# Kernel tuning notes

Measured on AMD Instinct MI355X. Metric: run time of the kernel, lower is better.

Reference implementation:

```python
import jax, jax.numpy as jnp
import numpy as np

# mamba-130m backbone dims. NOTE: the original torch code wires Conv1d(1,8,...) into a
# 768-d Mamba (a latent bug); we resolve it by making the downsample conv emit d_model.
B, L_IN = 2, 135000
D_MODEL, N_LAYERS = 768, 24
D_INNER, D_STATE, D_CONV, DT_RANK = 1536, 16, 4, 48
K_DS, S_DS = 32, 32
LATENT = 64


def setup_inputs() -> dict:
    key = jax.random.key(0)
    ks = jax.random.split(key, 16)
    s = 0.02
    dt = jax.random.uniform(ks[12], (N_LAYERS, D_INNER), minval=1e-3, maxval=1e-1)
    return {
        "x": jax.random.normal(ks[0], (B, 1, L_IN), dtype=jnp.float32),
        "conv_w": jax.random.normal(ks[1], (D_MODEL, 1, K_DS)) * s,
        "conv_b": jnp.zeros((D_MODEL,)),
        "norm_w": jnp.ones((N_LAYERS, D_MODEL)),
        "in_proj_w": jax.random.normal(ks[2], (N_LAYERS, 2 * D_INNER, D_MODEL)) * s,
        "conv1d_w": jax.random.normal(ks[3], (N_LAYERS, D_INNER, D_CONV)) * s,
        "conv1d_b": jnp.zeros((N_LAYERS, D_INNER)),
        "x_proj_w": jax.random.normal(ks[4], (N_LAYERS, DT_RANK + 2 * D_STATE, D_INNER)) * s,
        "dt_proj_w": jax.random.normal(ks[5], (N_LAYERS, D_INNER, DT_RANK)) * s,
        "dt_proj_b": dt + jnp.log(-jnp.expm1(-dt)),  # inverse-softplus init
        "A_log": jnp.log(jnp.broadcast_to(jnp.arange(1, D_STATE + 1, dtype=jnp.float32), (N_LAYERS, D_INNER, D_STATE)) + 0.0),
        "D_skip": jnp.ones((N_LAYERS, D_INNER)),
        "out_proj_w": jax.random.normal(ks[6], (N_LAYERS, D_MODEL, D_INNER)) * s,
        "norm_f_w": jnp.ones((D_MODEL,)),
        "proj_w": jax.random.normal(ks[7], (LATENT, D_MODEL)) * s,
        "proj_b": jnp.zeros((LATENT,)),
        "ln_w": jnp.ones((LATENT,)),
        "ln_b": jnp.zeros((LATENT,)),
    }


def _rmsnorm(x, w):
    return x * jax.lax.rsqrt(jnp.mean(x * x, axis=-1, keepdims=True) + 1e-5) * w


def _mamba_layer(h, p):
    norm_w, in_w, cw, cb, xp_w, dt_w, dt_b, A_log, Dp, out_w = p
    xz = jnp.einsum('btd,ed->bte', _rmsnorm(h, norm_w), in_w)  # e = 2*d_inner
    u, z = jnp.split(xz, 2, axis=-1)
    # causal depthwise conv over time
    uc = jax.lax.conv_general_dilated(jnp.transpose(u, (0, 2, 1)), cw[:, None, :], (1,),
                                      [(D_CONV - 1, 0)], dimension_numbers=('NCH', 'OIH', 'NCH'),
                                      feature_group_count=D_INNER)
    u = jax.nn.silu(jnp.transpose(uc + cb[None, :, None], (0, 2, 1)))  # (B,T,d_inner)
    proj = jnp.einsum('btd,ed->bte', u, xp_w)
    dt, Bm, Cm = jnp.split(proj, [DT_RANK, DT_RANK + D_STATE], axis=-1)
    delta = jax.nn.softplus(jnp.einsum('btr,dr->btd', dt, dt_w) + dt_b)
    A = -jnp.exp(A_log)  # (d_inner, d_state)

    def step(hc, inp):
        u_t, d_t, b_t, c_t = inp  # (B,d_inner),(B,d_inner),(B,d_state),(B,d_state)
        hc = jnp.exp(d_t[..., None] * A) * hc + (d_t * u_t)[..., None] * b_t[:, None, :]
        return hc, jnp.einsum('bds,bs->bd', hc, c_t)

    h0 = jnp.zeros((u.shape[0], D_INNER, D_STATE), dtype=u.dtype)
    tfirst = lambda a: jnp.transpose(a, (1, 0, 2))
    _, ys = jax.lax.scan(step, h0, (tfirst(u), tfirst(delta), tfirst(Bm), tfirst(Cm)))
    y = (jnp.transpose(ys, (1, 0, 2)) + u * Dp) * jax.nn.silu(z)
    return h + jnp.einsum('bte,de->btd', y, out_w), None


def _forward(x, conv_w, conv_b, norm_w, in_proj_w, conv1d_w, conv1d_b, x_proj_w, dt_proj_w,
             dt_proj_b, A_log, D_skip, out_proj_w, norm_f_w, proj_w, proj_b, ln_w, ln_b):
    # downsample: (B,1,135000) -> (B,768,4218) -> (B,4218,768)
    xds = jax.lax.conv_general_dilated(x, conv_w, (S_DS,), 'VALID',
                                       dimension_numbers=('NCH', 'OIH', 'NCH')) + conv_b[None, :, None]
    h = jnp.transpose(xds, (0, 2, 1))
    params = (norm_w, in_proj_w, conv1d_w, conv1d_b, x_proj_w, dt_proj_w, dt_proj_b, A_log, D_skip, out_proj_w)
    h, _ = jax.lax.scan(_mamba_layer, h, params)
    h = _rmsnorm(h, norm_f_w)  # last_hidden_state
    pooled = h.mean(axis=1)  # mean pooling
    zed = pooled @ proj_w.T + proj_b
    mu = zed.mean(-1, keepdims=True)
    var = ((zed - mu) ** 2).mean(-1, keepdims=True)
    return (zed - mu) * jax.lax.rsqrt(var + 1e-5) * ln_w + ln_b  # dropout is identity in eval


def reference(x, conv_w, conv_b, norm_w, in_proj_w, conv1d_w, conv1d_b, x_proj_w, dt_proj_w,
              dt_proj_b, A_log, D_skip, out_proj_w, norm_f_w, proj_w, proj_b, ln_w, ln_b):
    return _forward(x, conv_w, conv_b, norm_w, in_proj_w, conv1d_w, conv1d_b, x_proj_w,
                    dt_proj_w, dt_proj_b, A_log, D_skip, out_proj_w, norm_f_w, proj_w,
                    proj_b, ln_w, ln_b)
```

## Files before the change

### kernel.cpp

```cpp
#include <hip/hip_runtime.h>
#include <hip/hip_bf16.h>
#include <math.h>

#define TT 4218
#define BB 2
#define DM 768
#define DI 1536
#define DS 16
#define DTR 48
#define LC 64
#define NCHUNK 66
#define ROWS (BB*TT)
#define NLAYER 24

typedef short short8 __attribute__((ext_vector_type(8)));
typedef float f32x4 __attribute__((ext_vector_type(4)));

__device__ __forceinline__ float silu_f(float x) { return x / (1.0f + __expf(-x)); }
__device__ __forceinline__ float softplus_f(float x) {
  return (x > 15.0f) ? x : log1pf(__expf(x));
}
__device__ __forceinline__ unsigned short f2bf(float x) {
  unsigned int u = __float_as_uint(x);
  u = (u + 0x7fffu + ((u >> 16) & 1u)) >> 16;
  return (unsigned short)u;
}
__device__ __forceinline__ float bf2f(unsigned short s) {
  return __uint_as_float(((unsigned int)s) << 16);
}

__global__ __launch_bounds__(256)
void k_f2bf(const float4* __restrict__ in, ushort4* __restrict__ out, int n4) {
  int i = blockIdx.x*256 + threadIdx.x;
  if (i >= n4) return;
  float4 v = in[i];
  ushort4 o;
  o.x = f2bf(v.x); o.y = f2bf(v.y); o.z = f2bf(v.z); o.w = f2bf(v.w);
  out[i] = o;
}

__global__ __launch_bounds__(256)
void k_cvt_dtw(const float* __restrict__ in, unsigned short* __restrict__ out, int n) {
  int i = blockIdx.x*256 + threadIdx.x;
  if (i >= n) return;
  int col = i & 63, row = i >> 6;
  out[i] = (col < DTR) ? f2bf(in[row*DTR + col]) : (unsigned short)0;
}

__global__ __launch_bounds__(256)
void k_zero_dtpad(unsigned short* __restrict__ fdt) {
  int i = blockIdx.x*256 + threadIdx.x;
  if (i >= ROWS*16) return;
  int r = i >> 4, c = i & 15;
  fdt[(size_t)r*64 + DTR + c] = 0;
}

__global__ __launch_bounds__(256)
void k_conv_ds(const float* __restrict__ x, const float* __restrict__ cw,
               const float* __restrict__ cb, float* __restrict__ h) {
  int bt = blockIdx.x;
  int b = bt / TT, t = bt % TT;
  __shared__ float xs[32];
  int tid = threadIdx.x;
  if (tid < 32) xs[tid] = x[(size_t)b*135000 + (size_t)t*32 + tid];
  __syncthreads();
  for (int d = tid; d < DM; d += 256) {
    float s = cb[d];
    const float* w = cw + d*32;
    #pragma unroll
    for (int k = 0; k < 32; ++k) s = fmaf(xs[k], w[k], s);
    h[(size_t)bt*DM + d] = s;
  }
}

__global__ __launch_bounds__(256)
void k_rmsnorm(const float* __restrict__ in, const float* __restrict__ w,
               unsigned short* __restrict__ out) {
  int row = blockIdx.x, tid = threadIdx.x;
  const float* xp = in + (size_t)row*DM;
  float v0 = xp[tid], v1 = xp[tid+256], v2 = xp[tid+512];
  float ss = v0*v0 + v1*v1 + v2*v2;
  #pragma unroll
  for (int off = 32; off > 0; off >>= 1) ss += __shfl_down(ss, off, 64);
  __shared__ float sred[4];
  if ((tid & 63) == 0) sred[tid >> 6] = ss;
  __syncthreads();
  float tot = sred[0] + sred[1] + sred[2] + sred[3];
  float sc = rsqrtf(tot * (1.0f/DM) + 1e-5f);
  unsigned short* op = out + (size_t)row*DM;
  op[tid]     = f2bf(v0*sc*w[tid]);
  op[tid+256] = f2bf(v1*sc*w[tid+256]);
  op[tid+512] = f2bf(v2*sc*w[tid+512]);
}

#define GLL(g, l) __builtin_amdgcn_global_load_lds( \
    (const __attribute__((address_space(1))) void*)(g), \
    (__attribute__((address_space(3))) void*)(l), 16, 0, 0)

template<int MODE>
__global__ __launch_bounds__(256)
void k_gemm_bf(const unsigned short* __restrict__ A,
               const unsigned short* __restrict__ W,
               const float* __restrict__ bias,
               float* __restrict__ Cf,
               unsigned short* __restrict__ Cb0, unsigned short* __restrict__ Cb1,
               int ldc, int M, int N, int K) {
  __shared__ unsigned short As[128*32];
  __shared__ unsigned short Ws[128*32];
  const int tid = threadIdx.x;
  const int m0 = blockIdx.x*128, n0 = blockIdx.y*128;
  const int lane = tid & 63;
  const int wave = tid >> 6;
  const int wm = (wave >> 1)*64, wn = (wave & 1)*64;

  const int sA = tid & 3;
  const int r0 = tid >> 2;
  const int r1 = r0 + 64;
  const int seg0 = sA ^ ((r0 >> 1) & 3);
  const int seg1 = sA ^ ((r1 >> 1) & 3);
  const unsigned short* gA0 = A + (size_t)min(m0+r0, M-1)*K + seg0*8;
  const unsigned short* gA1 = A + (size_t)min(m0+r1, M-1)*K + seg1*8;
  const unsigned short* gW0 = W + (size_t)min(n0+r0, N-1)*K + seg0*8;
  const unsigned short* gW1 = W + (size_t)min(n0+r1, N-1)*K + seg1*8;
  unsigned short* lA0 = As + tid*8;
  unsigned short* lA1 = As + (tid+256)*8;
  unsigned short* lW0 = Ws + tid*8;
  unsigned short* lW1 = Ws + (tid+256)*8;

  f32x4 acc[4][4];
  #pragma unroll
  for (int i = 0; i < 4; ++i)
    #pragma unroll
    for (int j = 0; j < 4; ++j) acc[i][j] = (f32x4){0.f,0.f,0.f,0.f};

  const int lr = lane & 15, kg = lane >> 4;
  const int sw = (kg ^ ((lr >> 1) & 3)) * 8;
  const int aoff = (wm + lr)*32 + sw;
  const int boff = (wn + lr)*32 + sw;

  for (int k0 = 0; k0 < K; k0 += 32) {
    GLL(gA0, lA0); GLL(gA1, lA1);
    GLL(gW0, lW0); GLL(gW1, lW1);
    gA0 += 32; gA1 += 32; gW0 += 32; gW1 += 32;
    __syncthreads();
    short8 af[4], bfr[4];
    #pragma unroll
    for (int i = 0; i < 4; ++i) {
      af[i]  = *(const short8*)(As + aoff + i*512);
      bfr[i] = *(const short8*)(Ws + boff + i*512);
    }
    #pragma unroll
    for (int i = 0; i < 4; ++i)
      #pragma unroll
      for (int j = 0; j < 4; ++j)
        acc[i][j] = __builtin_amdgcn_mfma_f32_16x16x32_bf16(af[i], bfr[j], acc[i][j], 0, 0, 0);
    __syncthreads();
  }

  #pragma unroll
  for (int i = 0; i < 4; ++i) {
    int gr0 = m0 + wm + i*16 + kg*4;
    #pragma unroll
    for (int j = 0; j < 4; ++j) {
      int gc = n0 + wn + j*16 + lr;
      if (gc >= N) continue;
      #pragma unroll
      for (int r = 0; r < 4; ++r) {
        int gr = gr0 + r;
        if (gr >= M) continue;
        float v = acc[i][j][r];
        if (MODE == 0) {
          if (gc < DI) Cb0[(size_t)gr*ldc + gc] = f2bf(v);
          else         Cb1[(size_t)gr*ldc + gc - DI] = f2bf(v);
        } else if (MODE == 1) {
          Cf[(size_t)gr*ldc + gc] += v;
        } else {
          Cf[(size_t)gr*ldc + gc] = softplus_f(v + bias[gc]);
        }
      }
    }
  }
}

__global__ __launch_bounds__(256)
void k_gemm_xp(const unsigned short* __restrict__ A,
               const unsigned short* __restrict__ W,
               float* __restrict__ Cpr, unsigned short* __restrict__ Cdt,
               int M) {
  __shared__ unsigned short As[64*32];
  __shared__ unsigned short Ws[80*32];
  const int tid = threadIdx.x;
  const int m0 = blockIdx.x*64;
  const int lane = tid & 63;
  const int wave = tid >> 6;
  const int K = DI;

  const int rA = tid >> 2;
  const int segA = (tid & 3) ^ ((rA >> 1) & 3);
  const unsigned short* gA = A + (size_t)min(m0+rA, M-1)*K + segA*8;
  unsigned short* lA = As + tid*8;
  const int rW0 = tid >> 2;
  const int segW0 = (tid & 3) ^ ((rW0 >> 1) & 3);
  const unsigned short* gW0 = W + (size_t)rW0*K + segW0*8;
  unsigned short* lW0 = Ws + tid*8;
  const int idx1 = tid + 256;
  const int rW1 = idx1 >> 2;
  const int segW1 = (idx1 & 3) ^ ((rW1 >> 1) & 3);
  const unsigned short* gW1 = W + (size_t)min(rW1,79)*K + segW1*8;
  unsigned short* lW1 = Ws + (size_t)idx1*8;

  f32x4 acc[5];
  #pragma unroll
  for (int j = 0; j < 5; ++j) acc[j] = (f32x4){0.f,0.f,0.f,0.f};

  const int lr = lane & 15, kg = lane >> 4;
  const int sw = (kg ^ ((lr >> 1) & 3)) * 8;
  const int aoff = (wave*16 + lr)*32 + sw;

  for (int k0 = 0; k0 < K; k0 += 32) {
    GLL(gA, lA);
    GLL(gW0, lW0);
    if (wave == 0) GLL(gW1, lW1);
    gA += 32; gW0 += 32; gW1 += 32;
    __syncthreads();
    short8 af = *(const short8*)(As + aoff);
    #pragma unroll
    for (int j = 0; j < 5; ++j) {
      short8 bf = *(const short8*)(Ws + (j*16 + lr)*32 + sw);
      acc[j] = __builtin_amdgcn_mfma_f32_16x16x32_bf16(af, bf, acc[j], 0, 0, 0);
    }
    __syncthreads();
  }

  #pragma unroll
  for (int j = 0; j < 5; ++j) {
    int gc = j*16 + lr;
    #pragma unroll
    for (int r = 0; r < 4; ++r) {
      int gr = m0 + wave*16 + kg*4 + r;
      if (gr >= M) continue;
      float v = acc[j][r];
      Cpr[(size_t)gr*80 + gc] = v;
      if (gc < DTR) Cdt[(size_t)gr*64 + gc] = f2bf(v);
    }
  }
}

__global__ __launch_bounds__(256)
void k_dwconv(const unsigned short* __restrict__ U0, const float* __restrict__ cw,
              const float* __restrict__ cb, unsigned short* __restrict__ ubf) {
  size_t i = (size_t)blockIdx.x*256 + threadIdx.x;
  if (i >= (size_t)ROWS*DI) return;
  int d = (int)(i % DI);
  long bt = (long)(i / DI);
  int t = (int)(bt % TT);
  float s = cb[d];
  #pragma unroll
  for (int k = 0; k < 4; ++k) {
    int tt = t - 3 + k;
    if (tt >= 0) s = fmaf(bf2f(U0[(size_t)(bt - 3 + k)*DI + d]), cw[d*4 + k], s);
  }
  ubf[i] = f2bf(silu_f(s));
}

__global__ __launch_bounds__(256)
void k_scan1(const float* __restrict__ delta, const unsigned short* __restrict__ u,
             const float* __restrict__ proj, const float* __restrict__ A_log,
             float* __restrict__ P, float* __restrict__ H) {
  int c = blockIdx.x, b = blockIdx.z;
  int d = blockIdx.y * 256 + threadIdx.x;
  float A[DS];
  #pragma unroll
  for (int s = 0; s < DS; ++s) A[s] = -__expf(A_log[d*DS + s]);
  float h[DS] = {};
  float Pp[DS];
  #pragma unroll
  for (int s = 0; s < DS; ++s) Pp[s] = 1.0f;
  int t0 = c * LC, t1 = min(t0 + LC, TT);
  for (int t = t0; t < t1; ++t) {
    size_t bt = (size_t)b*TT + t;
    float dl = delta[bt*DI + d];
    float du = dl * bf2f(u[bt*DI + d]);
    const float* pbm = proj + bt*80 + DTR;
    #pragma unroll
    for (int s = 0; s < DS; ++s) {
      float e = __expf(dl * A[s]);
      Pp[s] *= e;
      h[s] = fmaf(e, h[s], du * pbm[s]);
    }
  }
  size_t o = (((size_t)c*BB + b)*DI + d)*DS;
  #pragma unroll
  for (int s = 0; s < DS; ++s) { P[o+s] = Pp[s]; H[o+s] = h[s]; }
}

__global__ __launch_bounds__(256)
void k_scan2(float* __restrict__ P, float* __restrict__ H) {
  int i = blockIdx.x*256 + threadIdx.x;
  const int CH = BB*DI*DS;
  float carry = 0.0f;
  for (int c = 0; c < NCHUNK; ++c) {
    size_t o = (size_t)c*CH + i;
    float p = P[o], h0 = H[o];
    H[o] = carry;
    carry = fmaf(p, carry, h0);
  }
}

__global__ __launch_bounds__(256)
void k_scan3(const float* __restrict__ delta, const unsigned short* __restrict__ u,
             const unsigned short* __restrict__ z, const float* __restrict__ proj,
             const float* __restrict__ A_log, const float* __restrict__ Dskip,
             const float* __restrict__ H, unsigned short* __restrict__ y) {
  int c = blockIdx.x, b = blockIdx.z;
  int d = blockIdx.y * 256 + threadIdx.x;
  float A[DS];
  #pragma unroll
  for (int s = 0; s < DS; ++s) A[s] = -__expf(A_log[d*DS + s]);
  float h[DS];
  size_t o = (((size_t)c*BB + b)*DI + d)*DS;
  #pragma unroll
  for (int s = 0; s < DS; ++s) h[s] = H[o+s];
  float Dd = Dskip[d];
  int t0 = c * LC, t1 = min(t0 + LC, TT);
  for (int t = t0; t < t1; ++t) {
    size_t bt = (size_t)b*TT + t;
    float dl = delta[bt*DI + d];
    float uu = bf2f(u[bt*DI + d]);
    float du = dl * uu;
    const float* pbm = proj + bt*80 + DTR;
    const float* pcm = pbm + DS;
    float yt = 0.0f;
    #pragma unroll
    for (int s = 0; s < DS; ++s) {
      float e = __expf(dl * A[s]);
      h[s] = fmaf(e, h[s], du * pbm[s]);
      yt = fmaf(h[s], pcm[s], yt);
    }
    float zz = bf2f(z[bt*DI + d]);
    y[bt*DI + d] = f2bf((yt + uu*Dd) * silu_f(zz));
  }
}

__global__ __launch_bounds__(256)
void k_poolpart(const unsigned short* __restrict__ hn, float* __restrict__ pp) {
  int seg = blockIdx.x, b = blockIdx.z;
  int d = blockIdx.y*256 + threadIdx.x;
  int t0 = seg*132, t1 = min(t0 + 132, TT);
  float s = 0.0f;
  for (int t = t0; t < t1; ++t) s += bf2f(hn[((size_t)b*TT + t)*DM + d]);
  pp[((size_t)b*32 + seg)*DM + d] = s;
}

__global__ __launch_bounds__(256)
void k_head(const float* __restrict__ pp, const float* __restrict__ pw,
            const float* __restrict__ pb, const float* __restrict__ lnw,
            const float* __restrict__ lnb, float* __restrict__ out) {
  int b = blockIdx.x, tid = threadIdx.x;
  __shared__ float pooled[DM];
  for (int d = tid; d < DM; d += 256) {
    float s = 0.0f;
    for (int seg = 0; seg < 32; ++seg) s += pp[((size_t)b*32 + seg)*DM + d];
    pooled[d] = s * (1.0f/(float)TT);
  }
  __syncthreads();
  __shared__ float zed[64];
  if (tid < 64) {
    float s = pb[tid];
    const float* w = pw + (size_t)tid*DM;
    for (int d = 0; d < DM; ++d) s = fmaf(pooled[d], w[d], s);
    zed[tid] = s;
  }
  __syncthreads();
  __shared__ float mv[2];
  if (tid == 0) {
    float mu = 0.0f;
    for (int l = 0; l < 64; ++l) mu += zed[l];
    mu *= (1.0f/64.0f);
    float var = 0.0f;
    for (int l = 0; l < 64; ++l) { float dd = zed[l]-mu; var += dd*dd; }
    var *= (1.0f/64.0f);
    mv[0] = mu; mv[1] = rsqrtf(var + 1e-5f);
  }
  __syncthreads();
  if (tid < 64) out[b*64 + tid] = (zed[tid]-mv[0])*mv[1]*lnw[tid] + lnb[tid];
}

extern "C" void kernel_launch(void* const* d_in, const int* in_sizes, int n_in,
                              void* d_out, int out_size, void* d_ws, size_t ws_size,
                              hipStream_t stream) {
  (void)in_sizes; (void)n_in; (void)out_size; (void)ws_size;
  const float* x    = (const float*)d_in[0];
  const float* cw   = (const float*)d_in[1];
  const float* cb   = (const float*)d_in[2];
  const float* nw   = (const float*)d_in[3];
  const float* inw  = (const float*)d_in[4];
  const float* c1w  = (const float*)d_in[5];
  const float* c1b  = (const float*)d_in[6];
  const float* xpw  = (const float*)d_in[7];
  const float* dtw  = (const float*)d_in[8];
  const float* dtb  = (const float*)d_in[9];
  const float* alog = (const float*)d_in[10];
  const float* dsk  = (const float*)d_in[11];
  const float* outw = (const float*)d_in[12];
  const float* nfw  = (const float*)d_in[13];
  const float* pw   = (const float*)d_in[14];
  const float* pb   = (const float*)d_in[15];
  const float* lnw  = (const float*)d_in[16];
  const float* lnb  = (const float*)d_in[17];

  char* wsb = (char*)d_ws;
  size_t o = 0;
  float* f_h  = (float*)(wsb + o); o += (size_t)ROWS*DM*4;
  float* f_pr = (float*)(wsb + o); o += (size_t)ROWS*80*4;
  float* f_dl = (float*)(wsb + o); o += (size_t)ROWS*DI*4;
  float* f_P  = (float*)(wsb + o); o += (size_t)NCHUNK*BB*DI*DS*4;
  float* f_H  = (float*)(wsb + o); o += (size_t)NCHUNK*BB*DI*DS*4;
  float* f_pp = (float*)(wsb + o); o += (size_t)BB*32*DM*4;
  unsigned short* hn_bf = (unsigned short*)(wsb + o); o += (size_t)ROWS*DM*2;
  unsigned short* u0_bf = (unsigned short*)(wsb + o); o += (size_t)ROWS*DI*2;
  unsigned short* z_bf  = (unsigned short*)(wsb + o); o += (size_t)ROWS*DI*2;
  unsigned short* u_bf  = (unsigned short*)(wsb + o); o += (size_t)ROWS*DI*2;
  unsigned short* y_bf  = (unsigned short*)(wsb + o); o += (size_t)ROWS*DI*2;
  unsigned short* f_dt  = (unsigned short*)(wsb + o); o += (size_t)ROWS*64*2;
  unsigned short* w_in  = (unsigned short*)(wsb + o); o += (size_t)2*DI*DM*2;
  unsigned short* w_xp  = (unsigned short*)(wsb + o); o += (size_t)NLAYER*80*DI*2;
  unsigned short* w_out = (unsigned short*)(wsb + o); o += (size_t)NLAYER*DM*DI*2;
  unsigned short* w_dt  = (unsigned short*)(wsb + o); o += (size_t)NLAYER*DI*64*2;

  k_conv_ds<<<ROWS, 256, 0, stream>>>(x, cw, cb, f_h);
  k_f2bf<<<(NLAYER*80*DI/4+255)/256, 256, 0, stream>>>(
      (const float4*)xpw, (ushort4*)w_xp, NLAYER*80*DI/4);
  k_f2bf<<<(NLAYER*DM*DI/4+255)/256, 256, 0, stream>>>(
      (const float4*)outw, (ushort4*)w_out, NLAYER*DM*DI/4);
  k_cvt_dtw<<<(NLAYER*DI*64+255)/256, 256, 0, stream>>>(dtw, w_dt, NLAYER*DI*64);
  k_zero_dtpad<<<(ROWS*16+255)/256, 256, 0, stream>>>(f_dt);

  for (int lay = 0; lay < NLAYER; ++lay) {
    k_f2bf<<<(2*DI*DM/4+255)/256, 256, 0, stream>>>(
        (const float4*)(inw + (size_t)lay*2*DI*DM), (ushort4*)w_in, 2*DI*DM/4);
    k_rmsnorm<<<ROWS, 256, 0, stream>>>(f_h, nw + (size_t)lay*DM, hn_bf);
    k_gemm_bf<0><<<dim3(66,24), 256, 0, stream>>>(
        hn_bf, w_in, nullptr, nullptr, u0_bf, z_bf, DI, ROWS, 2*DI, DM);
    k_dwconv<<<((size_t)ROWS*DI+255)/256, 256, 0, stream>>>(
        u0_bf, c1w + (size_t)lay*DI*4, c1b + (size_t)lay*DI, u_bf);
    k_gemm_xp<<<132, 256, 0, stream>>>(
        u_bf, w_xp + (size_t)lay*80*DI, f_pr, f_dt, ROWS);
    k_gemm_bf<2><<<dim3(66,12), 256, 0, stream>>>(
        f_dt, w_dt + (size_t)lay*DI*64, dtb + (size_t)lay*DI,
        f_dl, nullptr, nullptr, DI, ROWS, DI, 64);
    k_scan1<<<dim3(NCHUNK,6,BB), 256, 0, stream>>>(
        f_dl, u_bf, f_pr, alog + (size_t)lay*DI*DS, f_P, f_H);
    k_scan2<<<dim3((BB*DI*DS)/256), 256, 0, stream>>>(f_P, f_H);
    k_scan3<<<dim3(NCHUNK,6,BB), 256, 0, stream>>>(
        f_dl, u_bf, z_bf, f_pr, alog + (size_t)lay*DI*DS,
        dsk + (size_t)lay*DI, f_H, y_bf);
    k_gemm_bf<1><<<dim3(66,6), 256, 0, stream>>>(
        y_bf, w_out + (size_t)lay*DM*DI, nullptr,
        f_h, nullptr, nullptr, DM, ROWS, DM, DI);
  }

  k_rmsnorm<<<ROWS, 256, 0, stream>>>(f_h, nfw, hn_bf);
  k_poolpart<<<dim3(32,3,BB), 256, 0, stream>>>(hn_bf, f_pp);
  k_head<<<BB, 256, 0, stream>>>(f_pp, pw, pb, lnw, lnb, (float*)d_out);
}
```

Before: 11.12 ms.

## Vectorize scan and dwconv loads, widen xp GEMM K-tile, pad GEMM grids

Several unrelated micro-optimizations land together. The dwconv kernel now handles four channels per thread with vector loads, the scan kernels read B/C/A_log/H as float4, scan1 computes the chunk decay as exp(sum(dt)*A) instead of a running product, scan2 prefetches two chunks ahead, and the x_proj GEMM uses a 64-wide K tile with an 8-way XOR swizzle. The GEMM grids are enlarged to 72 row-blocks with an early exit for out-of-range blocks. The intent is fewer memory instructions and fewer barrier iterations, at the cost of more LDS in the xp GEMM and a slightly different rounding of the chunk decay.

```diff
diff --git a/kernel.cpp b/kernel.cpp
--- a/kernel.cpp
+++ b/kernel.cpp
@@ -105,10 +105,11 @@
                float* __restrict__ Cf,
                unsigned short* __restrict__ Cb0, unsigned short* __restrict__ Cb1,
                int ldc, int M, int N, int K) {
+  const int m0 = blockIdx.x*128, n0 = blockIdx.y*128;
+  if (m0 >= M) return;
   __shared__ unsigned short As[128*32];
   __shared__ unsigned short Ws[128*32];
   const int tid = threadIdx.x;
-  const int m0 = blockIdx.x*128, n0 = blockIdx.y*128;
   const int lane = tid & 63;
   const int wave = tid >> 6;
   const int wm = (wave >> 1)*64, wn = (wave & 1)*64;
@@ -187,47 +188,54 @@
                const unsigned short* __restrict__ W,
                float* __restrict__ Cpr, unsigned short* __restrict__ Cdt,
                int M) {
-  __shared__ unsigned short As[64*32];
-  __shared__ unsigned short Ws[80*32];
+  __shared__ unsigned short As[64*64];
+  __shared__ unsigned short Ws[80*64];
   const int tid = threadIdx.x;
   const int m0 = blockIdx.x*64;
   const int lane = tid & 63;
   const int wave = tid >> 6;
   const int K = DI;
 
-  const int rA = tid >> 2;
-  const int segA = (tid & 3) ^ ((rA >> 1) & 3);
-  const unsigned short* gA = A + (size_t)min(m0+rA, M-1)*K + segA*8;
-  unsigned short* lA = As + tid*8;
-  const int rW0 = tid >> 2;
-  const int segW0 = (tid & 3) ^ ((rW0 >> 1) & 3);
-  const unsigned short* gW0 = W + (size_t)rW0*K + segW0*8;
+  const int rA0 = tid >> 3,        gA0s = (tid & 7) ^ (rA0 & 7);
+  const int rA1 = (tid+256) >> 3,  gA1s = ((tid+256) & 7) ^ (rA1 & 7);
+  const unsigned short* gA0 = A + (size_t)min(m0+rA0, M-1)*K + gA0s*8;
+  const unsigned short* gA1 = A + (size_t)min(m0+rA1, M-1)*K + gA1s*8;
+  unsigned short* lA0 = As + tid*8;
+  unsigned short* lA1 = As + (size_t)(tid+256)*8;
+  const int rW0 = tid >> 3,        gW0s = (tid & 7) ^ (rW0 & 7);
+  const int rW1 = (tid+256) >> 3,  gW1s = ((tid+256) & 7) ^ (rW1 & 7);
+  const int rW2 = (tid+512) >> 3,  gW2s = ((tid+512) & 7) ^ (rW2 & 7);
+  const unsigned short* gW0 = W + (size_t)rW0*K + gW0s*8;
+  const unsigned short* gW1 = W + (size_t)rW1*K + gW1s*8;
+  const unsigned short* gW2 = W + (size_t)min(rW2,79)*K + gW2s*8;
   unsigned short* lW0 = Ws + tid*8;
-  const int idx1 = tid + 256;
-  const int rW1 = idx1 >> 2;
-  const int segW1 = (idx1 & 3) ^ ((rW1 >> 1) & 3);
-  const unsigned short* gW1 = W + (size_t)min(rW1,79)*K + segW1*8;
-  unsigned short* lW1 = Ws + (size_t)idx1*8;
+  unsigned short* lW1 = Ws + (size_t)(tid+256)*8;
+  unsigned short* lW2 = Ws + (size_t)(tid+512)*8;
+  const bool doW2 = (tid < 128);
 
   f32x4 acc[5];
   #pragma unroll
   for (int j = 0; j < 5; ++j) acc[j] = (f32x4){0.f,0.f,0.f,0.f};
 
   const int lr = lane & 15, kg = lane >> 4;
-  const int sw = (kg ^ ((lr >> 1) & 3)) * 8;
-  const int aoff = (wave*16 + lr)*32 + sw;
-
-  for (int k0 = 0; k0 < K; k0 += 32) {
-    GLL(gA, lA);
-    GLL(gW0, lW0);
-    if (wave == 0) GLL(gW1, lW1);
-    gA += 32; gW0 += 32; gW1 += 32;
+  const int rowA = wave*16 + lr;
+
+  for (int k0 = 0; k0 < K; k0 += 64) {
+    GLL(gA0, lA0); GLL(gA1, lA1);
+    GLL(gW0, lW0); GLL(gW1, lW1);
+    if (doW2) GLL(gW2, lW2);
+    gA0 += 64; gA1 += 64; gW0 += 64; gW1 += 64; gW2 += 64;
     __syncthreads();
-    short8 af = *(const short8*)(As + aoff);
-    #pragma unroll
-    for (int j = 0; j < 5; ++j) {
-      short8 bf = *(const short8*)(Ws + (j*16 + lr)*32 + sw);
-      acc[j] = __builtin_amdgcn_mfma_f32_16x16x32_bf16(af, bf, acc[j], 0, 0, 0);
+    #pragma unroll
+    for (int ks = 0; ks < 2; ++ks) {
+      const int G = ks*4 + kg;
+      short8 af = *(const short8*)(As + ((size_t)rowA*8 + (G ^ (rowA & 7)))*8);
+      #pragma unroll
+      for (int j = 0; j < 5; ++j) {
+        const int rw = j*16 + lr;
+        short8 bf = *(const short8*)(Ws + ((size_t)rw*8 + (G ^ (rw & 7)))*8);
+        acc[j] = __builtin_amdgcn_mfma_f32_16x16x32_bf16(af, bf, acc[j], 0, 0, 0);
+      }
     }
     __syncthreads();
   }
@@ -249,18 +257,36 @@
 __global__ __launch_bounds__(256)
 void k_dwconv(const unsigned short* __restrict__ U0, const float* __restrict__ cw,
               const float* __restrict__ cb, unsigned short* __restrict__ ubf) {
-  size_t i = (size_t)blockIdx.x*256 + threadIdx.x;
-  if (i >= (size_t)ROWS*DI) return;
-  int d = (int)(i % DI);
-  long bt = (long)(i / DI);
+  size_t i4 = (size_t)blockIdx.x*256 + threadIdx.x;
+  if (i4 >= (size_t)ROWS*DI/4) return;
+  size_t base = i4*4;
+  int d = (int)(base % DI);
+  size_t bt = base / DI;
   int t = (int)(bt % TT);
-  float s = cb[d];
+  float4 cbv = *(const float4*)(cb + d);
+  float s0 = cbv.x, s1 = cbv.y, s2 = cbv.z, s3 = cbv.w;
+  float4 w0v = *(const float4*)(cw + (size_t)(d+0)*4);
+  float4 w1v = *(const float4*)(cw + (size_t)(d+1)*4);
+  float4 w2v = *(const float4*)(cw + (size_t)(d+2)*4);
+  float4 w3v = *(const float4*)(cw + (size_t)(d+3)*4);
+  const float* w0 = (const float*)&w0v;
+  const float* w1 = (const float*)&w1v;
+  const float* w2 = (const float*)&w2v;
+  const float* w3 = (const float*)&w3v;
   #pragma unroll
   for (int k = 0; k < 4; ++k) {
     int tt = t - 3 + k;
-    if (tt >= 0) s = fmaf(bf2f(U0[(size_t)(bt - 3 + k)*DI + d]), cw[d*4 + k], s);
-  }
-  ubf[i] = f2bf(silu_f(s));
+    if (tt < 0) continue;
+    ushort4 uu = *(const ushort4*)(U0 + (bt - 3 + k)*DI + d);
+    s0 = fmaf(bf2f(uu.x), w0[k], s0);
+    s1 = fmaf(bf2f(uu.y), w1[k], s1);
+    s2 = fmaf(bf2f(uu.z), w2[k], s2);
+    s3 = fmaf(bf2f(uu.w), w3[k], s3);
+  }
+  ushort4 o4;
+  o4.x = f2bf(silu_f(s0)); o4.y = f2bf(silu_f(s1));
+  o4.z = f2bf(silu_f(s2)); o4.w = f2bf(silu_f(s3));
+  *(ushort4*)(ubf + base) = o4;
 }
 
 __global__ __launch_bounds__(256)
@@ -270,40 +296,60 @@
   int c = blockIdx.x, b = blockIdx.z;
   int d = blockIdx.y * 256 + threadIdx.x;
   float A[DS];
-  #pragma unroll
-  for (int s = 0; s < DS; ++s) A[s] = -__expf(A_log[d*DS + s]);
+  {
+    const float4* a4 = (const float4*)(A_log + (size_t)d*DS);
+    #pragma unroll
+    for (int q = 0; q < 4; ++q) {
+      float4 v = a4[q];
+      A[q*4+0] = -__expf(v.x); A[q*4+1] = -__expf(v.y);
+      A[q*4+2] = -__expf(v.z); A[q*4+3] = -__expf(v.w);
+    }
+  }
   float h[DS] = {};
-  float Pp[DS];
-  #pragma unroll
-  for (int s = 0; s < DS; ++s) Pp[s] = 1.0f;
+  float sdl = 0.0f;
   int t0 = c * LC, t1 = min(t0 + LC, TT);
   for (int t = t0; t < t1; ++t) {
     size_t bt = (size_t)b*TT + t;
     float dl = delta[bt*DI + d];
     float du = dl * bf2f(u[bt*DI + d]);
-    const float* pbm = proj + bt*80 + DTR;
+    const float4* pb4 = (const float4*)(proj + bt*80 + DTR);
+    float4 B0 = pb4[0], B1 = pb4[1], B2 = pb4[2], B3 = pb4[3];
+    float Bv[DS] = {B0.x,B0.y,B0.z,B0.w, B1.x,B1.y,B1.z,B1.w,
+                    B2.x,B2.y,B2.z,B2.w, B3.x,B3.y,B3.z,B3.w};
+    sdl += dl;
     #pragma unroll
     for (int s = 0; s < DS; ++s) {
       float e = __expf(dl * A[s]);
-      Pp[s] *= e;
-      h[s] = fmaf(e, h[s], du * pbm[s]);
+      h[s] = fmaf(e, h[s], du * Bv[s]);
     }
   }
   size_t o = (((size_t)c*BB + b)*DI + d)*DS;
   #pragma unroll
-  for (int s = 0; s < DS; ++s) { P[o+s] = Pp[s]; H[o+s] = h[s]; }
+  for (int q = 0; q < 4; ++q) {
+    float4 pv, hv;
+    pv.x = __expf(sdl*A[q*4+0]); pv.y = __expf(sdl*A[q*4+1]);
+    pv.z = __expf(sdl*A[q*4+2]); pv.w = __expf(sdl*A[q*4+3]);
+    hv.x = h[q*4+0]; hv.y = h[q*4+1]; hv.z = h[q*4+2]; hv.w = h[q*4+3];
+    *(float4*)(P + o + q*4) = pv;
+    *(float4*)(H + o + q*4) = hv;
+  }
 }
 
 __global__ __launch_bounds__(256)
 void k_scan2(float* __restrict__ P, float* __restrict__ H) {
   int i = blockIdx.x*256 + threadIdx.x;
-  const int CH = BB*DI*DS;
+  const size_t CH = (size_t)BB*DI*DS;
+  size_t o = (size_t)i;
   float carry = 0.0f;
+  float p0 = P[o],      h0 = H[o];
+  float p1 = P[o + CH], h1 = H[o + CH];
   for (int c = 0; c < NCHUNK; ++c) {
-    size_t o = (size_t)c*CH + i;
-    float p = P[o], h0 = H[o];
+    float p2 = 0.0f, h2 = 0.0f;
+    if (c + 2 < NCHUNK) { size_t o2 = o + 2*CH; p2 = P[o2]; h2 = H[o2]; }
     H[o] = carry;
-    carry = fmaf(p, carry, h0);
+    carry = fmaf(p0, carry, h0);
+    p0 = p1; h0 = h1; p1 = p2; h1 = h2;
+    o += CH;
   }
 }
 
@@ -315,12 +361,22 @@
   int c = blockIdx.x, b = blockIdx.z;
   int d = blockIdx.y * 256 + threadIdx.x;
   float A[DS];
-  #pragma unroll
-  for (int s = 0; s < DS; ++s) A[s] = -__expf(A_log[d*DS + s]);
+  {
+    const float4* a4 = (const float4*)(A_log + (size_t)d*DS);
+    #pragma unroll
+    for (int q = 0; q < 4; ++q) {
+      float4 v = a4[q];
+      A[q*4+0] = -__expf(v.x); A[q*4+1] = -__expf(v.y);
+      A[q*4+2] = -__expf(v.z); A[q*4+3] = -__expf(v.w);
+    }
+  }
   float h[DS];
   size_t o = (((size_t)c*BB + b)*DI + d)*DS;
   #pragma unroll
-  for (int s = 0; s < DS; ++s) h[s] = H[o+s];
+  for (int q = 0; q < 4; ++q) {
+    float4 hv = *(const float4*)(H + o + q*4);
+    h[q*4+0] = hv.x; h[q*4+1] = hv.y; h[q*4+2] = hv.z; h[q*4+3] = hv.w;
+  }
   float Dd = Dskip[d];
   int t0 = c * LC, t1 = min(t0 + LC, TT);
   for (int t = t0; t < t1; ++t) {
@@ -328,14 +384,19 @@
     float dl = delta[bt*DI + d];
     float uu = bf2f(u[bt*DI + d]);
     float du = dl * uu;
-    const float* pbm = proj + bt*80 + DTR;
-    const float* pcm = pbm + DS;
+    const float4* pb4 = (const float4*)(proj + bt*80 + DTR);
+    float4 B0 = pb4[0], B1 = pb4[1], B2 = pb4[2], B3 = pb4[3];
+    float4 C0 = pb4[4], C1 = pb4[5], C2 = pb4[6], C3 = pb4[7];
+    float Bv[DS] = {B0.x,B0.y,B0.z,B0.w, B1.x,B1.y,B1.z,B1.w,
+                    B2.x,B2.y,B2.z,B2.w, B3.x,B3.y,B3.z,B3.w};
+    float Cv[DS] = {C0.x,C0.y,C0.z,C0.w, C1.x,C1.y,C1.z,C1.w,
+                    C2.x,C2.y,C2.z,C2.w, C3.x,C3.y,C3.z,C3.w};
     float yt = 0.0f;
     #pragma unroll
     for (int s = 0; s < DS; ++s) {
       float e = __expf(dl * A[s]);
-      h[s] = fmaf(e, h[s], du * pbm[s]);
-      yt = fmaf(h[s], pcm[s], yt);
+      h[s] = fmaf(e, h[s], du * Bv[s]);
+      yt = fmaf(h[s], Cv[s], yt);
     }
     float zz = bf2f(z[bt*DI + d]);
     y[bt*DI + d] = f2bf((yt + uu*Dd) * silu_f(zz));
@@ -440,13 +501,13 @@
     k_f2bf<<<(2*DI*DM/4+255)/256, 256, 0, stream>>>(
         (const float4*)(inw + (size_t)lay*2*DI*DM), (ushort4*)w_in, 2*DI*DM/4);
     k_rmsnorm<<<ROWS, 256, 0, stream>>>(f_h, nw + (size_t)lay*DM, hn_bf);
-    k_gemm_bf<0><<<dim3(66,24), 256, 0, stream>>>(
+    k_gemm_bf<0><<<dim3(72,24), 256, 0, stream>>>(
         hn_bf, w_in, nullptr, nullptr, u0_bf, z_bf, DI, ROWS, 2*DI, DM);
-    k_dwconv<<<((size_t)ROWS*DI+255)/256, 256, 0, stream>>>(
+    k_dwconv<<<(int)(((size_t)ROWS*DI/4+255)/256), 256, 0, stream>>>(
         u0_bf, c1w + (size_t)lay*DI*4, c1b + (size_t)lay*DI, u_bf);
     k_gemm_xp<<<132, 256, 0, stream>>>(
         u_bf, w_xp + (size_t)lay*80*DI, f_pr, f_dt, ROWS);
-    k_gemm_bf<2><<<dim3(66,12), 256, 0, stream>>>(
+    k_gemm_bf<2><<<dim3(72,12), 256, 0, stream>>>(
         f_dt, w_dt + (size_t)lay*DI*64, dtb + (size_t)lay*DI,
         f_dl, nullptr, nullptr, DI, ROWS, DI, 64);
     k_scan1<<<dim3(NCHUNK,6,BB), 256, 0, stream>>>(
@@ -455,7 +516,7 @@
     k_scan3<<<dim3(NCHUNK,6,BB), 256, 0, stream>>>(
         f_dl, u_bf, z_bf, f_pr, alog + (size_t)lay*DI*DS,
         dsk + (size_t)lay*DI, f_H, y_bf);
-    k_gemm_bf<1><<<dim3(66,6), 256, 0, stream>>>(
+    k_gemm_bf<1><<<dim3(72,6), 256, 0, stream>>>(
         y_bf, w_out + (size_t)lay*DM*DI, nullptr,
         f_h, nullptr, nullptr, DM, ROWS, DM, DI);
   }
```

New measurement: 11.64 ms. +4.7%, slower.
